# Kernel tuning notes

Measured on AMD Instinct MI355X. Metric: run time of the kernel, lower is better.

## Reference

```python
import jax, jax.numpy as jnp
import numpy as np
import math

N_X, N_Y, N_Z, N_W = 25, 7, 6, 5
LEN_DATASET = 10000


def _trap_w(vals):
    # trapezoidal quadrature weights for a uniform grid
    dx = vals[1] - vals[0]
    return jnp.full(vals.shape, dx, vals.dtype).at[0].multiply(0.5).at[-1].multiply(0.5)


def setup_inputs() -> dict:
    key = jax.random.key(0)
    k1, k2 = jax.random.split(key, 2)
    x = jax.random.normal(k1, (5, 256, 256), jnp.float32)
    theta = jax.random.normal(k2, (1, 256, 256), jnp.float32) * 0.01
    grid = jnp.zeros((LEN_DATASET // 5, 5, N_X, N_Y, N_Z, N_W), jnp.float32)
    return {"x": x, "theta": theta, "grid": grid, "j": 3}


def reference(x, theta, grid, j):
    A = theta[0]  # [256,256]
    x_vals = jnp.linspace(0.0, 2.0 * math.pi, N_X)
    y_vals = jnp.linspace(-0.09, 0.09, N_Y)
    z_vals = jnp.linspace(-0.09, 0.09, N_Z)
    w_vals = jnp.linspace(0.9, 1.1, N_W)
    # separable trapezoidal weights -> [Nx,Ny,Nz,Nw]
    W4 = jnp.einsum('a,b,c,d->abcd', _trap_w(x_vals), _trap_w(y_vals),
                    _trap_w(z_vals), _trap_w(w_vals))
    # per-item projection onto theta (trap_int's data/parameter coupling)
    s = jnp.einsum('nij,ij->n', x, A)  # [5]
    arg = (s[:, None, None, None, None]
           * jnp.cos(x_vals)[None, :, None, None, None]
           * w_vals[None, None, None, None, :]
           + y_vals[None, None, :, None, None]
           + z_vals[None, None, None, :, None])
    f_grid = jnp.exp(-arg * arg)  # [5,Nx,Ny,Nz,Nw]
    # trapezoidal integral per item, summed over the batch
    loss = jnp.sum(f_grid * W4[None]) - 0.5 * jnp.sum(jnp.abs(theta))
    grid_new = grid.at[j].set(f_grid)  # persistent buffer scatter write
    return loss, theta[0], grid_new
```

## Files before the change

### kernel.cpp

```cpp
#include <hip/hip_runtime.h>
#include <math.h>

#define NPTS   65536
#define NB     5
#define NX     25
#define NY     7
#define NZ     6
#define NW     5
#define FG     (NB*NX*NY*NZ*NW)
#define GRID_ELEMS (2000 * FG)
#define NCHUNKM ((GRID_ELEMS - 4) / 4)

typedef float float4a __attribute__((ext_vector_type(4), aligned(4)));
typedef float float4v __attribute__((ext_vector_type(4), aligned(16)));

__device__ __forceinline__ float fgrid_eval(const float* s, int e2, float* w4out) {
    const float PI2 = 6.283185307179586f;
    const float dxs = PI2 / 24.0f;
    const float dys = 0.03f;
    const float dzs = 0.036f;
    const float dws = 0.05f;
    int d  = e2 % NW;
    int cz = (e2 / NW) % NZ;
    int b  = (e2 / (NW * NZ)) % NY;
    int a  = (e2 / (NW * NZ * NY)) % NX;
    int n  = e2 / (NW * NZ * NY * NX);
    float xv = PI2 * (float)a / 24.0f;
    float cv = cosf(xv);
    float yv = -0.09f + dys * (float)b;
    float zv = -0.09f + dzs * (float)cz;
    float wv = 0.9f  + dws * (float)d;
    float arg = s[n] * cv * wv + yv + zv;
    float f = expf(-arg * arg);
    *w4out = dxs * ((a == 0 || a == NX - 1) ? 0.5f : 1.0f)
           * dys * ((b == 0 || b == NY - 1) ? 0.5f : 1.0f)
           * dzs * ((cz == 0 || cz == NZ - 1) ? 0.5f : 1.0f)
           * dws * ((d == 0 || d == NW - 1) ? 0.5f : 1.0f);
    return f;
}

__global__ void reduce_kernel(const float* __restrict__ x,
                              const float* __restrict__ theta,
                              float* __restrict__ out_theta,
                              float* __restrict__ ws) {
    __shared__ float smem[4 * 6];
    int idx = blockIdx.x * blockDim.x + threadIdx.x;
    float t = theta[idx];
    out_theta[idx] = t;

    float vals[6];
#pragma unroll
    for (int n = 0; n < 5; ++n) vals[n] = x[n * NPTS + idx] * t;
    vals[5] = fabsf(t);

    int lane = threadIdx.x & 63;
    int wave = threadIdx.x >> 6;
#pragma unroll
    for (int k = 0; k < 6; ++k) {
        float v = vals[k];
#pragma unroll
        for (int off = 32; off > 0; off >>= 1) v += __shfl_down(v, off, 64);
        if (lane == 0) smem[wave * 6 + k] = v;
    }
    __syncthreads();
    if (threadIdx.x < 6) {
        float acc = smem[threadIdx.x] + smem[6 + threadIdx.x] +
                    smem[12 + threadIdx.x] + smem[18 + threadIdx.x];
        atomicAdd(&ws[threadIdx.x], acc);
    }
}

__global__ void __launch_bounds__(256)
copy_fgrid_kernel(const float* __restrict__ grid,
                  float* __restrict__ out_grid,
                  const float* __restrict__ ws_in,
                  float* __restrict__ ws_out,
                  const int* __restrict__ jptr) {
    const int j = *jptr;
    const int jlo = j * FG;
    const int jhi = jlo + FG;

    float s[5];
#pragma unroll
    for (int n = 0; n < 5; ++n) s[n] = ws_in[n];

    float local = 0.0f;
    const long long t = (long long)blockIdx.x * blockDim.x + threadIdx.x;

    if (t < NCHUNKM) {
        const int e0 = 3 + 4 * (int)t;
        float4a v = *(const float4a*)(grid + e0);
        if (e0 + 3 >= jlo && e0 < jhi) {
#pragma unroll
            for (int q = 0; q < 4; ++q) {
                int e = e0 + q;
                if (e >= jlo && e < jhi) {
                    float w4;
                    float f = fgrid_eval(s, e - jlo, &w4);
                    v[q] = f;
                    local += f * w4;
                }
            }
        }
        float4v vv = {v[0], v[1], v[2], v[3]};
        __builtin_nontemporal_store(vv, (float4v*)(out_grid + e0));
    }

    if (t == 0) {
        const int edges[4] = {0, 1, 2, GRID_ELEMS - 1};
#pragma unroll
        for (int k = 0; k < 4; ++k) {
            int e = edges[k];
            float val;
            if (e >= jlo && e < jhi) {
                float w4;
                val = fgrid_eval(s, e - jlo, &w4);
                local += val * w4;
            } else {
                val = grid[e];
            }
            out_grid[e] = val;
        }
    }

#pragma unroll
    for (int off = 32; off > 0; off >>= 1) local += __shfl_down(local, off, 64);
    if ((threadIdx.x & 63) == 0 && local != 0.0f) atomicAdd(&ws_out[6], local);
}

__global__ void finalize_kernel(const float* __restrict__ ws,
                                float* __restrict__ out) {
    out[0] = ws[6] - 0.5f * ws[5];
}

extern "C" void kernel_launch(void* const* d_in, const int* in_sizes, int n_in,
                              void* d_out, int out_size, void* d_ws, size_t ws_size,
                              hipStream_t stream) {
    const float* x     = (const float*)d_in[0];
    const float* theta = (const float*)d_in[1];
    const float* grid  = (const float*)d_in[2];
    const int*   jptr  = (const int*)d_in[3];

    float* out = (float*)d_out;
    float* ws  = (float*)d_ws;

    hipMemsetAsync(ws, 0, 7 * sizeof(float), stream);

    reduce_kernel<<<NPTS / 256, 256, 0, stream>>>(x, theta, out + 1, ws);

    const int nblk = (NCHUNKM + 255) / 256;
    copy_fgrid_kernel<<<nblk, 256, 0, stream>>>(grid, out + 1 + NPTS,
                                                ws, ws, jptr);

    finalize_kernel<<<1, 1, 0, stream>>>(ws, out);
}
```

Measured before the change: 362.9 us.

## Split grid copy from f_grid scatter and process four chunks per thread

Splits the fused copy-and-evaluate kernel into a plain bulk copy kernel and a small f_grid kernel that overwrites slice j afterward. The copy kernel now handles four float4 chunks per thread, with all loads issued before the stores, to raise memory-level parallelism and remove per-element range checks. The f_grid kernel reduces across the block before issuing one atomic per block. In exchange, slice j is written twice and there is an extra launch.

```diff
diff --git a/kernel.cpp b/kernel.cpp
--- a/kernel.cpp
+++ b/kernel.cpp
@@ -10,6 +10,7 @@
 #define FG     (NB*NX*NY*NZ*NW)
 #define GRID_ELEMS (2000 * FG)
 #define NCHUNKM ((GRID_ELEMS - 4) / 4)
+#define CHUNKS_PER_BLOCK 1024
 
 typedef float float4a __attribute__((ext_vector_type(4), aligned(4)));
 typedef float float4v __attribute__((ext_vector_type(4), aligned(16)));
@@ -71,61 +72,59 @@
 }
 
 __global__ void __launch_bounds__(256)
-copy_fgrid_kernel(const float* __restrict__ grid,
-                  float* __restrict__ out_grid,
-                  const float* __restrict__ ws_in,
-                  float* __restrict__ ws_out,
-                  const int* __restrict__ jptr) {
-    const int j = *jptr;
-    const int jlo = j * FG;
-    const int jhi = jlo + FG;
+copy_kernel(const float* __restrict__ grid,
+            float* __restrict__ out_grid) {
+    const long long base = (long long)blockIdx.x * CHUNKS_PER_BLOCK + threadIdx.x;
+    float4v v[4];
+    long long c[4];
+#pragma unroll
+    for (int k = 0; k < 4; ++k) {
+        c[k] = base + (long long)k * 256;
+        if (c[k] < NCHUNKM) {
+            float4a t = *(const float4a*)(grid + 3 + 4 * c[k]);
+            v[k] = (float4v){t[0], t[1], t[2], t[3]};
+        }
+    }
+#pragma unroll
+    for (int k = 0; k < 4; ++k) {
+        if (c[k] < NCHUNKM)
+            __builtin_nontemporal_store(v[k], (float4v*)(out_grid + 3 + 4 * c[k]));
+    }
+    if (blockIdx.x == 0 && threadIdx.x == 0) {
+        out_grid[0] = grid[0];
+        out_grid[1] = grid[1];
+        out_grid[2] = grid[2];
+        out_grid[GRID_ELEMS - 1] = grid[GRID_ELEMS - 1];
+    }
+}
+
+__global__ void __launch_bounds__(256)
+fgrid_kernel(const float* __restrict__ ws_in,
+             float* __restrict__ ws_out,
+             const int* __restrict__ jptr,
+             float* __restrict__ out_grid) {
+    __shared__ float smem[4];
+    const int e = blockIdx.x * 256 + threadIdx.x;
 
     float s[5];
 #pragma unroll
     for (int n = 0; n < 5; ++n) s[n] = ws_in[n];
+    const int j = *jptr;
 
     float local = 0.0f;
-    const long long t = (long long)blockIdx.x * blockDim.x + threadIdx.x;
-
-    if (t < NCHUNKM) {
-        const int e0 = 3 + 4 * (int)t;
-        float4a v = *(const float4a*)(grid + e0);
-        if (e0 + 3 >= jlo && e0 < jhi) {
-#pragma unroll
-            for (int q = 0; q < 4; ++q) {
-                int e = e0 + q;
-                if (e >= jlo && e < jhi) {
-                    float w4;
-                    float f = fgrid_eval(s, e - jlo, &w4);
-                    v[q] = f;
-                    local += f * w4;
-                }
-            }
-        }
-        float4v vv = {v[0], v[1], v[2], v[3]};
-        __builtin_nontemporal_store(vv, (float4v*)(out_grid + e0));
+    if (e < FG) {
+        float w4;
+        float f = fgrid_eval(s, e, &w4);
+        out_grid[(long long)j * FG + e] = f;
+        local = f * w4;
     }
-
-    if (t == 0) {
-        const int edges[4] = {0, 1, 2, GRID_ELEMS - 1};
-#pragma unroll
-        for (int k = 0; k < 4; ++k) {
-            int e = edges[k];
-            float val;
-            if (e >= jlo && e < jhi) {
-                float w4;
-                val = fgrid_eval(s, e - jlo, &w4);
-                local += val * w4;
-            } else {
-                val = grid[e];
-            }
-            out_grid[e] = val;
-        }
-    }
-
 #pragma unroll
     for (int off = 32; off > 0; off >>= 1) local += __shfl_down(local, off, 64);
-    if ((threadIdx.x & 63) == 0 && local != 0.0f) atomicAdd(&ws_out[6], local);
+    int lane = threadIdx.x & 63, wave = threadIdx.x >> 6;
+    if (lane == 0) smem[wave] = local;
+    __syncthreads();
+    if (threadIdx.x == 0)
+        atomicAdd(&ws_out[6], smem[0] + smem[1] + smem[2] + smem[3]);
 }
 
 __global__ void finalize_kernel(const float* __restrict__ ws,
@@ -148,9 +147,11 @@
 
     reduce_kernel<<<NPTS / 256, 256, 0, stream>>>(x, theta, out + 1, ws);
 
-    const int nblk = (NCHUNKM + 255) / 256;
-    copy_fgrid_kernel<<<nblk, 256, 0, stream>>>(grid, out + 1 + NPTS,
-                                                ws, ws, jptr);
+    const int nblk = (NCHUNKM + CHUNKS_PER_BLOCK - 1) / CHUNKS_PER_BLOCK;
+    copy_kernel<<<nblk, 256, 0, stream>>>(grid, out + 1 + NPTS);
+
+    fgrid_kernel<<<(FG + 255) / 256, 256, 0, stream>>>(ws, ws, jptr,
+                                                       out + 1 + NPTS);
 
     finalize_kernel<<<1, 1, 0, stream>>>(ws, out);
 }
```

Result: slower. 383.2 us (+5.6%).
